# Kernel tuning notes

Hardware: AMD Instinct MI355X
Metric: run time of the kernel (lower is better)

Reference implementation:

```python
import math
import jax, jax.numpy as jnp
import numpy as np

NUM_HEADS = 8
DEPTH = 1
LAMBDA_INIT = 0.8 - 0.6 * math.exp(-0.3 * DEPTH)
EPS = 1e-5


def setup_inputs() -> dict:
    key = jax.random.key(0)
    ks = jax.random.split(key, 10)
    B, C, H, W = 2, 256, 48, 48
    hd = C // NUM_HEADS
    return {
        "x": jax.random.normal(ks[0], (B, C, H, W), jnp.float32),
        "q_w": jax.random.normal(ks[1], (2 * C, C), jnp.float32) * (C ** -0.5),
        "k_w": jax.random.normal(ks[2], (2 * C, C), jnp.float32) * (C ** -0.5),
        "v_w": jax.random.normal(ks[3], (2 * C, C), jnp.float32) * (C ** -0.5),
        "out_w": jax.random.normal(ks[4], (C, 2 * C), jnp.float32) * ((2 * C) ** -0.5),
        "lambda_q1": 0.1 * jax.random.normal(ks[5], (NUM_HEADS, hd), jnp.float32),
        "lambda_k1": 0.1 * jax.random.normal(ks[6], (NUM_HEADS, hd), jnp.float32),
        "lambda_q2": 0.1 * jax.random.normal(ks[7], (NUM_HEADS, hd), jnp.float32),
        "lambda_k2": 0.1 * jax.random.normal(ks[8], (NUM_HEADS, hd), jnp.float32),
        "rms_scale": jnp.ones((1, 1, 2 * hd), jnp.float32),
    }


def reference(x, q_w, k_w, v_w, out_w, lambda_q1, lambda_k1, lambda_q2, lambda_k2, rms_scale):
    B, C, H, W = x.shape
    nh = NUM_HEADS
    hd = C // nh          # per-branch head dim
    N = H * W
    xf = x.reshape(B, C, N)

    def proj(w):
        # 1x1 conv == channel matmul; then split heads: (B, nh, 2*hd, N) -> (B, nh, N, 2*hd)
        t = jnp.einsum('oc,bcn->bon', w, xf)
        return t.reshape(B, nh, 2 * hd, N).transpose(0, 1, 3, 2)

    Q = proj(q_w)
    K = proj(k_w)
    V = proj(v_w)          # (B, nh, N, 2*hd)
    Q1, Q2 = Q[..., :hd], Q[..., hd:]
    K1, K2 = K[..., :hd], K[..., hd:]

    scale = hd ** -0.5
    attn1 = jax.nn.softmax(jnp.einsum('bhnd,bhmd->bhnm', Q1, K1) * scale, axis=-1)
    attn2 = jax.nn.softmax(jnp.einsum('bhnd,bhmd->bhnm', Q2, K2) * scale, axis=-1)

    lam1 = jnp.exp(jnp.sum(lambda_q1 * lambda_k1, axis=-1))  # (nh,)
    lam2 = jnp.exp(jnp.sum(lambda_q2 * lambda_k2, axis=-1))
    lam = (lam1 - lam2 + LAMBDA_INIT)[None, :, None, None]

    out = jnp.einsum('bhnm,bhmd->bhnd', attn1 - lam * attn2, V)  # (B, nh, N, 2*hd)

    # fused RMSNorm over the 2*hd channel dim + scale + (1 - lambda_init)
    rms = jnp.sqrt(jnp.mean(out * out, axis=-1, keepdims=True) + EPS)
    out = out / rms * rms_scale.reshape(1, 1, 1, 2 * hd)
    out = out * (1.0 - LAMBDA_INIT)

    # (B, nh, N, 2*hd) -> (B, nh, 2*hd, N) -> (B, 2*C, H, W), then out 1x1 conv
    out = out.transpose(0, 1, 3, 2).reshape(B, 2 * C, N)
    y = jnp.einsum('oc,bcn->bon', out_w, out)
    return y.reshape(B, C, H, W)
```

## Files before the change

kernel.cpp:

```cpp
#include <hip/hip_runtime.h>
#include <math.h>

#define NH 8
#define HD 32
#define D2 64
#define CIN 256
#define NPIX 2304
#define PLANE ((size_t)2359296)
#define LAMBDA_INIT 0.35550906759096927f
#define ONE_MINUS_LI 0.6444909324090307f
#define SFC 0.25503491f

typedef __bf16 bf16x8 __attribute__((ext_vector_type(8)));
typedef float f32x4 __attribute__((ext_vector_type(4)));

__device__ __forceinline__ float4 ld4(const float* p) {
    return *reinterpret_cast<const float4*>(p);
}

__global__ __launch_bounds__(256) void proj_kernel(
    const float* __restrict__ x, const float* __restrict__ qw,
    const float* __restrict__ kw, const float* __restrict__ vw,
    __bf16* __restrict__ qkv)
{
    __shared__ __align__(16) float smem[2 * 32 * 132];
    float (*Wt)[132] = reinterpret_cast<float(*)[132]>(smem);
    float (*Xt)[132] = reinterpret_cast<float(*)[132]>(smem + 32 * 132);
    const int b = blockIdx.z & 1;
    const int p = blockIdx.z >> 1;
    const float* __restrict__ w = (p == 0) ? qw : ((p == 1) ? kw : vw);
    const int o0 = blockIdx.y * 128;
    const int n0 = blockIdx.x * 128;
    const int t = threadIdx.x;
    const int to = t >> 4, tn = t & 15;
    const float* __restrict__ xb = x + (size_t)b * CIN * NPIX;

    float acc[8][8];
    #pragma unroll
    for (int i = 0; i < 8; ++i)
        #pragma unroll
        for (int j = 0; j < 8; ++j) acc[i][j] = 0.f;

    for (int kc = 0; kc < CIN; kc += 32) {
        #pragma unroll
        for (int jj = 0; jj < 4; ++jj) {
            int f = t + jj * 256;
            int row = f >> 3, cq = f & 7;
            float4 wv = ld4(&w[(size_t)(o0 + row) * CIN + kc + cq * 4]);
            Wt[cq * 4 + 0][row] = wv.x;
            Wt[cq * 4 + 1][row] = wv.y;
            Wt[cq * 4 + 2][row] = wv.z;
            Wt[cq * 4 + 3][row] = wv.w;
        }
        #pragma unroll
        for (int jj = 0; jj < 4; ++jj) {
            int f = t + jj * 256;
            int c = f >> 5, nq = f & 31;
            float4 xv = ld4(&xb[(size_t)(kc + c) * NPIX + n0 + nq * 4]);
            *reinterpret_cast<float4*>(&Xt[c][nq * 4]) = xv;
        }
        __syncthreads();
        #pragma unroll 8
        for (int kk = 0; kk < 32; ++kk) {
            float4 wa = ld4(&Wt[kk][to * 8]);
            float4 wb = ld4(&Wt[kk][to * 8 + 4]);
            float4 xa = ld4(&Xt[kk][tn * 4]);
            float4 xc = ld4(&Xt[kk][tn * 4 + 64]);
            float wr[8] = {wa.x, wa.y, wa.z, wa.w, wb.x, wb.y, wb.z, wb.w};
            float xr[8] = {xa.x, xa.y, xa.z, xa.w, xc.x, xc.y, xc.z, xc.w};
            #pragma unroll
            for (int i = 0; i < 8; ++i)
                #pragma unroll
                for (int j = 0; j < 8; ++j)
                    acc[i][j] = fmaf(wr[i], xr[j], acc[i][j]);
        }
        __syncthreads();
    }

    __bf16* rb = reinterpret_cast<__bf16*>(smem);
    if (p < 2) {
        const float osc = (p == 0) ? SFC : 1.0f;
        #pragma unroll
        for (int j = 0; j < 8; ++j) {
            int nl = tn * 4 + ((j >> 2) << 6) + (j & 3);
            bf16x8 pk;
            #pragma unroll
            for (int i = 0; i < 8; ++i) pk[i] = (__bf16)(acc[i][j] * osc);
            *reinterpret_cast<bf16x8*>(rb + nl * 128 + to * 8) = pk;
        }
        __syncthreads();
        __bf16* gbase = qkv + (size_t)p * PLANE;
        #pragma unroll
        for (int pass = 0; pass < 8; ++pass) {
            int run = pass * 32 + (t >> 3);
            int cc = t & 7;
            int nl = run & 127, half = run >> 7;
            int hh = (o0 >> 6) + half;
            bf16x8 v = *reinterpret_cast<const bf16x8*>(rb + nl * 128 + half * 64 + cc * 8);
            *reinterpret_cast<bf16x8*>(
                gbase + ((size_t)(b * NH + hh) * NPIX + n0 + nl) * D2 + cc * 8) = v;
        }
    } else {
        #pragma unroll
        for (int i = 0; i < 8; ++i) {
            #pragma unroll
            for (int j = 0; j < 8; ++j) {
                int nl = tn * 4 + ((j >> 2) << 6) + (j & 3);
                int np = (nl & ~31) + 2 * (nl & 15) + ((nl >> 4) & 1);
                rb[(to * 8 + i) * 128 + np] = (__bf16)acc[i][j];
            }
        }
        __syncthreads();
        __bf16* gbase = qkv + 2 * PLANE;
        #pragma unroll
        for (int pass = 0; pass < 8; ++pass) {
            int row = pass * 16 + (t >> 4);
            int cc = t & 15;
            int o = o0 + row;
            int hh = o >> 6, d = o & 63;
            bf16x8 v = *reinterpret_cast<const bf16x8*>(rb + row * 128 + cc * 8);
            *reinterpret_cast<bf16x8*>(
                gbase + ((size_t)(b * NH + hh) * D2 + d) * NPIX + n0 + cc * 8) = v;
        }
    }
}


#define LOADK(KT, K0, K1, K2, K3)                                          \
    { const __bf16* kb_ = Kp + (size_t)((KT) + c) * D2 + g * 8;            \
      K0 = *(const bf16x8*)(kb_);                                          \
      K1 = *(const bf16x8*)(kb_ + 16 * D2);                                \
      K2 = *(const bf16x8*)(kb_ + 32);                                     \
      K3 = *(const bf16x8*)(kb_ + 16 * D2 + 32); }

#define SCORES(K0, K1, K2, K3, BUF)                                        \
    { const f32x4 zero_ = {0.f, 0.f, 0.f, 0.f};                            \
      f32x4 s10 = __builtin_amdgcn_mfma_f32_16x16x32_bf16(aq1, K0, zero_, 0, 0, 0); \
      f32x4 s11 = __builtin_amdgcn_mfma_f32_16x16x32_bf16(aq1, K1, zero_, 0, 0, 0); \
      f32x4 s20 = __builtin_amdgcn_mfma_f32_16x16x32_bf16(aq2, K2, zero_, 0, 0, 0); \
      f32x4 s21 = __builtin_amdgcn_mfma_f32_16x16x32_bf16(aq2, K3, zero_, 0, 0, 0); \
      unsigned char* pw1_ = pb + (BUF) * 2560;                             \
      unsigned char* pw2_ = pw1_ + 1280;                                   \
      _Pragma("unroll")                                                    \
      for (int r_ = 0; r_ < 4; ++r_) {                                     \
          float pa_ = __builtin_amdgcn_exp2f(s10[r_]);                     \
          float pc_ = __builtin_amdgcn_exp2f(s11[r_]);                     \
          __bf16 ba_ = (__bf16)pa_, bc_ = (__bf16)pc_;                     \
          unsigned int pk_ = (unsigned int)__builtin_bit_cast(unsigned short, ba_) \
                           | ((unsigned int)__builtin_bit_cast(unsigned short, bc_) << 16); \
          *(unsigned int*)(pw1_ + wr_off + r_ * 80) = pk_;                 \
          float qa_ = __builtin_amdgcn_exp2f(s20[r_]);                     \
          float qc_ = __builtin_amdgcn_exp2f(s21[r_]);                     \
          __bf16 bb_ = (__bf16)qa_, bd_ = (__bf16)qc_;                     \
          unsigned int qk_ = (unsigned int)__builtin_bit_cast(unsigned short, bb_) \
                           | ((unsigned int)__builtin_bit_cast(unsigned short, bd_) << 16); \
          *(unsigned int*)(pw2_ + wr_off + r_ * 80) = qk_;                 \
      } }

#define LOADV(KT, V0, V1, V2, V3)                                          \
    { const __bf16* vb_ = Vp + (size_t)c * NPIX + (KT) + g * 8;            \
      V0 = *(const bf16x8*)(vb_);                                          \
      V1 = *(const bf16x8*)(vb_ + (size_t)16 * NPIX);                      \
      V2 = *(const bf16x8*)(vb_ + (size_t)32 * NPIX);                      \
      V3 = *(const bf16x8*)(vb_ + (size_t)48 * NPIX); }

#define PVACC(PA1, PA2, V0, V1, V2, V3)                                    \
    { O1[0] = __builtin_amdgcn_mfma_f32_16x16x32_bf16(PA1, V0, O1[0], 0, 0, 0); \
      O1[1] = __builtin_amdgcn_mfma_f32_16x16x32_bf16(PA1, V1, O1[1], 0, 0, 0); \
      O1[2] = __builtin_amdgcn_mfma_f32_16x16x32_bf16(PA1, V2, O1[2], 0, 0, 0); \
      O1[3] = __builtin_amdgcn_mfma_f32_16x16x32_bf16(PA1, V3, O1[3], 0, 0, 0); \
      O1[4] = __builtin_amdgcn_mfma_f32_16x16x32_bf16(PA1, vone, O1[4], 0, 0, 0); \
      O2[0] = __builtin_amdgcn_mfma_f32_16x16x32_bf16(PA2, V0, O2[0], 0, 0, 0); \
      O2[1] = __builtin_amdgcn_mfma_f32_16x16x32_bf16(PA2, V1, O2[1], 0, 0, 0); \
      O2[2] = __builtin_amdgcn_mfma_f32_16x16x32_bf16(PA2, V2, O2[2], 0, 0, 0); \
      O2[3] = __builtin_amdgcn_mfma_f32_16x16x32_bf16(PA2, V3, O2[3], 0, 0, 0); \
      O2[4] = __builtin_amdgcn_mfma_f32_16x16x32_bf16(PA2, vone, O2[4], 0, 0, 0); }

__global__ __launch_bounds__(256) void attn_kernel(
    const __bf16* __restrict__ qkv,
    const float* __restrict__ lq1, const float* __restrict__ lk1,
    const float* __restrict__ lq2, const float* __restrict__ lk2,
    const float* __restrict__ rms_scale,
    float* __restrict__ ao)
{
    __shared__ __align__(16) unsigned char plds[4][2][2][1280];
    const int t = threadIdx.x;
    const int w = t >> 6, lane = t & 63;
    const int g = lane >> 4, c = lane & 15;
    const int bh = blockIdx.y, h = bh & 7;
    const int q0 = blockIdx.x * 16;
    const __bf16* __restrict__ Qp = qkv + (size_t)bh * NPIX * D2;
    const __bf16* __restrict__ Kp = qkv + PLANE + (size_t)bh * NPIX * D2;
    const __bf16* __restrict__ Vp = qkv + 2 * PLANE + (size_t)bh * D2 * NPIX;

    const bf16x8 aq1 = *(const bf16x8*)(Qp + (size_t)(q0 + c) * D2 + g * 8);
    const bf16x8 aq2 = *(const bf16x8*)(Qp + (size_t)(q0 + c) * D2 + 32 + g * 8);

    bf16x8 vone;
    #pragma unroll
    for (int j = 0; j < 8; ++j) vone[j] = (__bf16)1.0f;

    f32x4 O1[5], O2[5];
    #pragma unroll
    for (int i = 0; i < 5; ++i) {
        O1[i] = (f32x4){0.f, 0.f, 0.f, 0.f};
        O2[i] = (f32x4){0.f, 0.f, 0.f, 0.f};
    }

    unsigned char* pb = &plds[w][0][0][0];
    const int wr_off = (4 * g) * 80 + c * 4;
    const int rd_off = c * 80 + g * 16;

    bf16x8 ka0, ka1, ka2, ka3, kb0, kb1, kb2, kb3;

    LOADK(w * 32, ka0, ka1, ka2, ka3);
    SCORES(ka0, ka1, ka2, ka3, 0);
    LOADK(w * 32 + 128, ka0, ka1, ka2, ka3);

    for (int i = 0; i < 17; ++i) {
        const int kt_cur = (i * 4 + w) * 32;
        const int tpp = (i + 2 < 18) ? (i + 2) : 17;
        LOADK((tpp * 4 + w) * 32, kb0, kb1, kb2, kb3);
        unsigned char* pr1 = pb + (i & 1) * 2560;
        unsigned char* pr2 = pr1 + 1280;
        bf16x8 pa1 = *(const bf16x8*)(pr1 + rd_off);
        bf16x8 pa2 = *(const bf16x8*)(pr2 + rd_off);
        bf16x8 bv0, bv1, bv2, bv3;
        LOADV(kt_cur, bv0, bv1, bv2, bv3);
        SCORES(ka0, ka1, ka2, ka3, (i + 1) & 1);
        PVACC(pa1, pa2, bv0, bv1, bv2, bv3);
        ka0 = kb0; ka1 = kb1; ka2 = kb2; ka3 = kb3;
    }
    {
        const int kt_cur = (17 * 4 + w) * 32;
        unsigned char* pr1 = pb + 2560;
        unsigned char* pr2 = pr1 + 1280;
        bf16x8 pa1 = *(const bf16x8*)(pr1 + rd_off);
        bf16x8 pa2 = *(const bf16x8*)(pr2 + rd_off);
        bf16x8 bv0, bv1, bv2, bv3;
        LOADV(kt_cur, bv0, bv1, bv2, bv3);
        PVACC(pa1, pa2, bv0, bv1, bv2, bv3);
    }

    __syncthreads();
    float* comb = (float*)&plds[0][0][0][0];
    if (w > 0) {
        #pragma unroll
        for (int i = 0; i < 5; ++i)
            *(f32x4*)(comb + ((w - 1) * 5 + i) * 256 + lane * 4) = O1[i];
    }
    __syncthreads();
    if (w == 0) {
        #pragma unroll
        for (int i = 0; i < 5; ++i)
            #pragma unroll
            for (int ww = 0; ww < 3; ++ww)
                O1[i] += *(const f32x4*)(comb + (ww * 5 + i) * 256 + lane * 4);
    }
    __syncthreads();
    if (w > 0) {
        #pragma unroll
        for (int i = 0; i < 5; ++i)
            *(f32x4*)(comb + ((w - 1) * 5 + i) * 256 + lane * 4) = O2[i];
    }
    __syncthreads();
    if (w == 0) {
        #pragma unroll
        for (int i = 0; i < 5; ++i)
            #pragma unroll
            for (int ww = 0; ww < 3; ++ww)
                O2[i] += *(const f32x4*)(comb + (ww * 5 + i) * 256 + lane * 4);

        float la = 0.f, lb = 0.f;
        #pragma unroll 8
        for (int i = 0; i < HD; ++i) {
            la = fmaf(lq1[h * HD + i], lk1[h * HD + i], la);
            lb = fmaf(lq2[h * HD + i], lk2[h * HD + i], lb);
        }
        const float lam = __expf(la) - __expf(lb) + LAMBDA_INIT;

        float rs[4];
        #pragma unroll
        for (int ds = 0; ds < 4; ++ds) rs[ds] = rms_scale[ds * 16 + c];

        #pragma unroll
        for (int r = 0; r < 4; ++r) {
            int q = q0 + 4 * g + r;
            float inv1 = 1.f / O1[4][r];
            float w2 = lam / O2[4][r];
            float o0_ = O1[0][r] * inv1 - O2[0][r] * w2;
            float o1_ = O1[1][r] * inv1 - O2[1][r] * w2;
            float o2_ = O1[2][r] * inv1 - O2[2][r] * w2;
            float o3_ = O1[3][r] * inv1 - O2[3][r] * w2;
            float ss = o0_ * o0_ + o1_ * o1_ + o2_ * o2_ + o3_ * o3_;
            ss += __shfl_xor(ss, 1); ss += __shfl_xor(ss, 2);
            ss += __shfl_xor(ss, 4); ss += __shfl_xor(ss, 8);
            float invr = rsqrtf(ss * (1.f / 64.f) + 1e-5f) * ONE_MINUS_LI;
            float* dst = ao + ((size_t)bh * NPIX + q) * D2 + c;
            dst[0]  = o0_ * invr * rs[0];
            dst[16] = o1_ * invr * rs[1];
            dst[32] = o2_ * invr * rs[2];
            dst[48] = o3_ * invr * rs[3];
        }
    }
}

__global__ __launch_bounds__(128) void outproj_kernel(
    const float* __restrict__ ow, const float* __restrict__ ao,
    float* __restrict__ y)
{
    const int t = threadIdx.x;
    const int w = t >> 6, lane = t & 63;
    const int g = lane >> 4, c = lane & 15;
    const int b = blockIdx.z;
    const int o0 = blockIdx.y * 32 + w * 16;
    const int n0 = blockIdx.x * 64;

    f32x4 O[4];
    #pragma unroll
    for (int i = 0; i < 4; ++i) O[i] = (f32x4){0.f, 0.f, 0.f, 0.f};

    const float* __restrict__ owr = ow + (size_t)(o0 + c) * 512;
    const float* __restrict__ aob = ao + (size_t)b * NH * NPIX * D2;

    for (int ks = 0; ks < 16; ++ks) {
        const int k0 = ks * 32 + g * 8;
        float4 a0 = ld4(owr + k0);
        float4 a1 = ld4(owr + k0 + 4);
        bf16x8 af;
        af[0] = (__bf16)a0.x; af[1] = (__bf16)a0.y;
        af[2] = (__bf16)a0.z; af[3] = (__bf16)a0.w;
        af[4] = (__bf16)a1.x; af[5] = (__bf16)a1.y;
        af[6] = (__bf16)a1.z; af[7] = (__bf16)a1.w;
        const int hh = k0 >> 6, d = k0 & 63;
        const float* bbase = aob + (size_t)hh * NPIX * D2 + d;
        #pragma unroll
        for (int nt = 0; nt < 4; ++nt) {
            const float* bp = bbase + (size_t)(n0 + nt * 16 + c) * D2;
            float4 b0 = ld4(bp);
            float4 b1 = ld4(bp + 4);
            bf16x8 bf_;
            bf_[0] = (__bf16)b0.x; bf_[1] = (__bf16)b0.y;
            bf_[2] = (__bf16)b0.z; bf_[3] = (__bf16)b0.w;
            bf_[4] = (__bf16)b1.x; bf_[5] = (__bf16)b1.y;
            bf_[6] = (__bf16)b1.z; bf_[7] = (__bf16)b1.w;
            O[nt] = __builtin_amdgcn_mfma_f32_16x16x32_bf16(af, bf_, O[nt], 0, 0, 0);
        }
    }
    #pragma unroll
    for (int nt = 0; nt < 4; ++nt) {
        #pragma unroll
        for (int r = 0; r < 4; ++r) {
            y[((size_t)(b * 256 + o0 + 4 * g + r)) * NPIX + n0 + nt * 16 + c] = O[nt][r];
        }
    }
}

extern "C" void kernel_launch(void* const* d_in, const int* in_sizes, int n_in,
                              void* d_out, int out_size, void* d_ws, size_t ws_size,
                              hipStream_t stream) {
    (void)in_sizes; (void)n_in; (void)out_size; (void)ws_size;
    const float* x   = (const float*)d_in[0];
    const float* qw  = (const float*)d_in[1];
    const float* kw  = (const float*)d_in[2];
    const float* vw  = (const float*)d_in[3];
    const float* ow  = (const float*)d_in[4];
    const float* lq1 = (const float*)d_in[5];
    const float* lk1 = (const float*)d_in[6];
    const float* lq2 = (const float*)d_in[7];
    const float* lk2 = (const float*)d_in[8];
    const float* rs  = (const float*)d_in[9];
    float* out = (float*)d_out;
    __bf16* qkv = (__bf16*)d_ws;
    float* ao = (float*)(qkv + 3 * PLANE);

    proj_kernel<<<dim3(18, 4, 6), 256, 0, stream>>>(x, qw, kw, vw, qkv);
    attn_kernel<<<dim3(144, 16), 256, 0, stream>>>(qkv, lq1, lk1, lq2, lk2, rs, ao);
    outproj_kernel<<<dim3(36, 8, 2), 128, 0, stream>>>(ow, ao, out);
}
```

Before: 308.8 us.

## Keep softmax probabilities in registers by transposing score MFMA and permuting V layout

The score MFMA now computes the transposed product (K as A operand, Q as B), so each lane's exp2 outputs already form the A-operand fragment for the PV MFMA. This removes the LDS round-trip for probabilities. To keep the key ordering consistent, the projection kernel writes V with a new pixel permutation within each 32-pixel chunk. The explicit K double-buffer prefetch pipeline is dropped in favour of a simple loop unrolled by 2, which leaves load latency hiding to the compiler and wave scheduling.

```diff
diff --git a/kernel.cpp b/kernel.cpp
--- a/kernel.cpp
+++ b/kernel.cpp
@@ -106,7 +106,8 @@
             #pragma unroll
             for (int j = 0; j < 8; ++j) {
                 int nl = tn * 4 + ((j >> 2) << 6) + (j & 3);
-                int np = (nl & ~31) + 2 * (nl & 15) + ((nl >> 4) & 1);
+                int o = nl & 31;
+                int np = (nl & ~31) + ((o & 12) << 1) + ((o >> 4) << 2) + (o & 3);
                 rb[(to * 8 + i) * 128 + np] = (__bf16)acc[i][j];
             }
         }
@@ -125,57 +126,6 @@
     }
 }
 
-
-#define LOADK(KT, K0, K1, K2, K3)                                          \
-    { const __bf16* kb_ = Kp + (size_t)((KT) + c) * D2 + g * 8;            \
-      K0 = *(const bf16x8*)(kb_);                                          \
-      K1 = *(const bf16x8*)(kb_ + 16 * D2);                                \
-      K2 = *(const bf16x8*)(kb_ + 32);                                     \
-      K3 = *(const bf16x8*)(kb_ + 16 * D2 + 32); }
-
-#define SCORES(K0, K1, K2, K3, BUF)                                        \
-    { const f32x4 zero_ = {0.f, 0.f, 0.f, 0.f};                            \
-      f32x4 s10 = __builtin_amdgcn_mfma_f32_16x16x32_bf16(aq1, K0, zero_, 0, 0, 0); \
-      f32x4 s11 = __builtin_amdgcn_mfma_f32_16x16x32_bf16(aq1, K1, zero_, 0, 0, 0); \
-      f32x4 s20 = __builtin_amdgcn_mfma_f32_16x16x32_bf16(aq2, K2, zero_, 0, 0, 0); \
-      f32x4 s21 = __builtin_amdgcn_mfma_f32_16x16x32_bf16(aq2, K3, zero_, 0, 0, 0); \
-      unsigned char* pw1_ = pb + (BUF) * 2560;                             \
-      unsigned char* pw2_ = pw1_ + 1280;                                   \
-      _Pragma("unroll")                                                    \
-      for (int r_ = 0; r_ < 4; ++r_) {                                     \
-          float pa_ = __builtin_amdgcn_exp2f(s10[r_]);                     \
-          float pc_ = __builtin_amdgcn_exp2f(s11[r_]);                     \
-          __bf16 ba_ = (__bf16)pa_, bc_ = (__bf16)pc_;                     \
-          unsigned int pk_ = (unsigned int)__builtin_bit_cast(unsigned short, ba_) \
-                           | ((unsigned int)__builtin_bit_cast(unsigned short, bc_) << 16); \
-          *(unsigned int*)(pw1_ + wr_off + r_ * 80) = pk_;                 \
-          float qa_ = __builtin_amdgcn_exp2f(s20[r_]);                     \
-          float qc_ = __builtin_amdgcn_exp2f(s21[r_]);                     \
-          __bf16 bb_ = (__bf16)qa_, bd_ = (__bf16)qc_;                     \
-          unsigned int qk_ = (unsigned int)__builtin_bit_cast(unsigned short, bb_) \
-                           | ((unsigned int)__builtin_bit_cast(unsigned short, bd_) << 16); \
-          *(unsigned int*)(pw2_ + wr_off + r_ * 80) = qk_;                 \
-      } }
-
-#define LOADV(KT, V0, V1, V2, V3)                                          \
-    { const __bf16* vb_ = Vp + (size_t)c * NPIX + (KT) + g * 8;            \
-      V0 = *(const bf16x8*)(vb_);                                          \
-      V1 = *(const bf16x8*)(vb_ + (size_t)16 * NPIX);                      \
-      V2 = *(const bf16x8*)(vb_ + (size_t)32 * NPIX);                      \
-      V3 = *(const bf16x8*)(vb_ + (size_t)48 * NPIX); }
-
-#define PVACC(PA1, PA2, V0, V1, V2, V3)                                    \
-    { O1[0] = __builtin_amdgcn_mfma_f32_16x16x32_bf16(PA1, V0, O1[0], 0, 0, 0); \
-      O1[1] = __builtin_amdgcn_mfma_f32_16x16x32_bf16(PA1, V1, O1[1], 0, 0, 0); \
-      O1[2] = __builtin_amdgcn_mfma_f32_16x16x32_bf16(PA1, V2, O1[2], 0, 0, 0); \
-      O1[3] = __builtin_amdgcn_mfma_f32_16x16x32_bf16(PA1, V3, O1[3], 0, 0, 0); \
-      O1[4] = __builtin_amdgcn_mfma_f32_16x16x32_bf16(PA1, vone, O1[4], 0, 0, 0); \
-      O2[0] = __builtin_amdgcn_mfma_f32_16x16x32_bf16(PA2, V0, O2[0], 0, 0, 0); \
-      O2[1] = __builtin_amdgcn_mfma_f32_16x16x32_bf16(PA2, V1, O2[1], 0, 0, 0); \
-      O2[2] = __builtin_amdgcn_mfma_f32_16x16x32_bf16(PA2, V2, O2[2], 0, 0, 0); \
-      O2[3] = __builtin_amdgcn_mfma_f32_16x16x32_bf16(PA2, V3, O2[3], 0, 0, 0); \
-      O2[4] = __builtin_amdgcn_mfma_f32_16x16x32_bf16(PA2, vone, O2[4], 0, 0, 0); }
-
 __global__ __launch_bounds__(256) void attn_kernel(
     const __bf16* __restrict__ qkv,
     const float* __restrict__ lq1, const float* __restrict__ lk1,
@@ -183,7 +133,7 @@
     const float* __restrict__ rms_scale,
     float* __restrict__ ao)
 {
-    __shared__ __align__(16) unsigned char plds[4][2][2][1280];
+    __shared__ __align__(16) float comb[3840];
     const int t = threadIdx.x;
     const int w = t >> 6, lane = t & 63;
     const int g = lane >> 4, c = lane & 15;
@@ -207,43 +157,48 @@
         O2[i] = (f32x4){0.f, 0.f, 0.f, 0.f};
     }
 
-    unsigned char* pb = &plds[w][0][0][0];
-    const int wr_off = (4 * g) * 80 + c * 4;
-    const int rd_off = c * 80 + g * 16;
-
-    bf16x8 ka0, ka1, ka2, ka3, kb0, kb1, kb2, kb3;
-
-    LOADK(w * 32, ka0, ka1, ka2, ka3);
-    SCORES(ka0, ka1, ka2, ka3, 0);
-    LOADK(w * 32 + 128, ka0, ka1, ka2, ka3);
-
-    for (int i = 0; i < 17; ++i) {
-        const int kt_cur = (i * 4 + w) * 32;
-        const int tpp = (i + 2 < 18) ? (i + 2) : 17;
-        LOADK((tpp * 4 + w) * 32, kb0, kb1, kb2, kb3);
-        unsigned char* pr1 = pb + (i & 1) * 2560;
-        unsigned char* pr2 = pr1 + 1280;
-        bf16x8 pa1 = *(const bf16x8*)(pr1 + rd_off);
-        bf16x8 pa2 = *(const bf16x8*)(pr2 + rd_off);
-        bf16x8 bv0, bv1, bv2, bv3;
-        LOADV(kt_cur, bv0, bv1, bv2, bv3);
-        SCORES(ka0, ka1, ka2, ka3, (i + 1) & 1);
-        PVACC(pa1, pa2, bv0, bv1, bv2, bv3);
-        ka0 = kb0; ka1 = kb1; ka2 = kb2; ka3 = kb3;
-    }
-    {
-        const int kt_cur = (17 * 4 + w) * 32;
-        unsigned char* pr1 = pb + 2560;
-        unsigned char* pr2 = pr1 + 1280;
-        bf16x8 pa1 = *(const bf16x8*)(pr1 + rd_off);
-        bf16x8 pa2 = *(const bf16x8*)(pr2 + rd_off);
-        bf16x8 bv0, bv1, bv2, bv3;
-        LOADV(kt_cur, bv0, bv1, bv2, bv3);
-        PVACC(pa1, pa2, bv0, bv1, bv2, bv3);
+    #pragma unroll 2
+    for (int i = 0; i < 18; ++i) {
+        const int kt = (i * 4 + w) * 32;
+        const __bf16* kb = Kp + (size_t)(kt + c) * D2 + g * 8;
+        bf16x8 k10 = *(const bf16x8*)(kb);
+        bf16x8 k11 = *(const bf16x8*)(kb + 16 * D2);
+        bf16x8 k20 = *(const bf16x8*)(kb + 32);
+        bf16x8 k21 = *(const bf16x8*)(kb + 16 * D2 + 32);
+        const __bf16* vb = Vp + (size_t)c * NPIX + kt + g * 8;
+        bf16x8 v0 = *(const bf16x8*)(vb);
+        bf16x8 v1 = *(const bf16x8*)(vb + (size_t)16 * NPIX);
+        bf16x8 v2 = *(const bf16x8*)(vb + (size_t)32 * NPIX);
+        bf16x8 v3 = *(const bf16x8*)(vb + (size_t)48 * NPIX);
+
+        const f32x4 zero = {0.f, 0.f, 0.f, 0.f};
+        f32x4 s10 = __builtin_amdgcn_mfma_f32_16x16x32_bf16(k10, aq1, zero, 0, 0, 0);
+        f32x4 s11 = __builtin_amdgcn_mfma_f32_16x16x32_bf16(k11, aq1, zero, 0, 0, 0);
+        f32x4 s20 = __builtin_amdgcn_mfma_f32_16x16x32_bf16(k20, aq2, zero, 0, 0, 0);
+        f32x4 s21 = __builtin_amdgcn_mfma_f32_16x16x32_bf16(k21, aq2, zero, 0, 0, 0);
+
+        bf16x8 pa1, pa2;
+        #pragma unroll
+        for (int r = 0; r < 4; ++r) {
+            pa1[r]     = (__bf16)__builtin_amdgcn_exp2f(s10[r]);
+            pa1[4 + r] = (__bf16)__builtin_amdgcn_exp2f(s11[r]);
+            pa2[r]     = (__bf16)__builtin_amdgcn_exp2f(s20[r]);
+            pa2[4 + r] = (__bf16)__builtin_amdgcn_exp2f(s21[r]);
+        }
+
+        O1[0] = __builtin_amdgcn_mfma_f32_16x16x32_bf16(pa1, v0, O1[0], 0, 0, 0);
+        O1[1] = __builtin_amdgcn_mfma_f32_16x16x32_bf16(pa1, v1, O1[1], 0, 0, 0);
+        O1[2] = __builtin_amdgcn_mfma_f32_16x16x32_bf16(pa1, v2, O1[2], 0, 0, 0);
+        O1[3] = __builtin_amdgcn_mfma_f32_16x16x32_bf16(pa1, v3, O1[3], 0, 0, 0);
+        O1[4] = __builtin_amdgcn_mfma_f32_16x16x32_bf16(pa1, vone, O1[4], 0, 0, 0);
+        O2[0] = __builtin_amdgcn_mfma_f32_16x16x32_bf16(pa2, v0, O2[0], 0, 0, 0);
+        O2[1] = __builtin_amdgcn_mfma_f32_16x16x32_bf16(pa2, v1, O2[1], 0, 0, 0);
+        O2[2] = __builtin_amdgcn_mfma_f32_16x16x32_bf16(pa2, v2, O2[2], 0, 0, 0);
+        O2[3] = __builtin_amdgcn_mfma_f32_16x16x32_bf16(pa2, v3, O2[3], 0, 0, 0);
+        O2[4] = __builtin_amdgcn_mfma_f32_16x16x32_bf16(pa2, vone, O2[4], 0, 0, 0);
     }
 
     __syncthreads();
-    float* comb = (float*)&plds[0][0][0][0];
     if (w > 0) {
         #pragma unroll
         for (int i = 0; i < 5; ++i)
```

Measured after the change: 308.4 us. About the same (-0.1%).
